# Optimization experiments

Measured on AMD Instinct MI355X. Metric: run time of the kernel, lower is better.

The kernel has to match this reference:

```python
import jax, jax.numpy as jnp
import numpy as np

N = 100000      # nodes
E = 50000       # hyperedges
NNZ = 1600000   # nonzeros in incidence matrix (avg 16 nodes/hyperedge)
C = 128         # in_channels
H = 256         # hidden_size


def setup_inputs() -> dict:
    key = jax.random.key(0)
    ks = jax.random.split(key, 8)
    x = jax.random.normal(ks[0], (N, C), dtype=jnp.float32)
    inc_rows = jax.random.randint(ks[1], (NNZ,), 0, E, dtype=jnp.int32)
    inc_cols = jax.random.randint(ks[2], (NNZ,), 0, N, dtype=jnp.int32)
    inc_vals = jax.random.uniform(ks[3], (NNZ,), dtype=jnp.float32)
    y = jax.random.randint(ks[4], (N,), 0, 10, dtype=jnp.int32)
    batch_0 = jnp.zeros((N,), dtype=jnp.int32)
    # Linear params (PyTorch Linear: y = x @ W.T + b; we store W pre-transposed as [C,H])
    s = 1.0 / np.sqrt(C)
    W0 = jax.random.uniform(ks[5], (C, H), dtype=jnp.float32, minval=-s, maxval=s)
    b0 = jnp.zeros((H,), dtype=jnp.float32)
    W1 = jax.random.uniform(ks[6], (C, H), dtype=jnp.float32, minval=-s, maxval=s)
    b1 = jnp.zeros((H,), dtype=jnp.float32)
    return {"x": x, "inc_rows": inc_rows, "inc_cols": inc_cols, "inc_vals": inc_vals,
            "y": y, "batch_0": batch_0, "W0": W0, "b0": b0, "W1": W1, "b1": b1}


def reference(x, inc_rows, inc_cols, inc_vals, y, batch_0, W0, b0, W1, b1):
    # sparse incidence @ x : gather node features per nnz, scale, scatter-add into hyperedges
    gathered = x[inc_cols] * inc_vals[:, None]                     # [NNZ, C]
    x1 = jax.ops.segment_sum(gathered, inc_rows, num_segments=E)   # [E, C]
    x0_out = jax.nn.relu(x @ W0 + b0)    # [N, H]
    x1_out = jax.nn.relu(x1 @ W1 + b1)   # [E, H]
    return (y, batch_0, x0_out, x1_out)
```

## Files before the change

kernel.cpp:

```cpp
#include <hip/hip_runtime.h>

#define N_NODES 100000
#define E_EDGES 50000
#define NNZ_CNT 1600000
#define C_IN 128
#define H_OUT 256
#define BKT 128
#define NB 391
#define RPB 4096

typedef __attribute__((ext_vector_type(8))) short short8;
typedef __attribute__((ext_vector_type(4))) float f32x4;

__device__ __forceinline__ ushort f2b(float f) {
  union { float f; uint u; } v; v.f = f;
  return (ushort)((v.u + 0x7FFFu + ((v.u >> 16) & 1u)) >> 16);
}
__device__ __forceinline__ float b2f(ushort u) {
  union { uint u; float f; } v; v.u = ((uint)u) << 16;
  return v.f;
}

__global__ __launch_bounds__(256) void init_kernel(
    const float* __restrict__ x, const int* __restrict__ y,
    const int* __restrict__ batch0, ushort* __restrict__ xb,
    float* __restrict__ out, int* __restrict__ chist, int nconv4) {
  int i = blockIdx.x * 256 + threadIdx.x;
  if (i < nconv4) {
    float4 v = ((const float4*)x)[i];
    ushort4 u;
    u.x = f2b(v.x); u.y = f2b(v.y); u.z = f2b(v.z); u.w = f2b(v.w);
    ((ushort4*)xb)[i] = u;
  }
  if (i < NB) chist[i] = 0;
  if (i < N_NODES) {
    out[i]           = (float)y[i];
    out[N_NODES + i] = (float)batch0[i];
  }
}

__global__ __launch_bounds__(256) void histc_kernel(
    const int* __restrict__ rows, int* __restrict__ chist) {
  __shared__ int h[NB];
  int t = threadIdx.x;
  for (int b = t; b < NB; b += 256) h[b] = 0;
  __syncthreads();
  int i0 = blockIdx.x * RPB;
  for (int k = 0; k < RPB / 256; ++k) {
    int i = i0 + k * 256 + t;
    if (i < NNZ_CNT) atomicAdd(&h[rows[i] >> 7], 1);
  }
  __syncthreads();
  for (int b = t; b < NB; b += 256)
    if (h[b]) atomicAdd(&chist[b], h[b]);
}

__global__ __launch_bounds__(512) void scanc_kernel(
    const int* __restrict__ chist, int* __restrict__ boff,
    int* __restrict__ gtail, int* __restrict__ eoff) {
  __shared__ int s[512];
  int t = threadIdx.x;
  int v = (t < NB) ? chist[t] : 0;
  s[t] = v;
  __syncthreads();
  for (int d = 1; d < 512; d <<= 1) {
    int u = (t >= d) ? s[t - d] : 0;
    __syncthreads();
    s[t] += u;
    __syncthreads();
  }
  if (t < NB) {
    int ex = s[t] - v;
    boff[t]  = ex;
    gtail[t] = ex;
  }
  if (t == 0) { boff[NB] = NNZ_CNT; eoff[NB * BKT] = NNZ_CNT; }
}

__global__ __launch_bounds__(256) void binpass_kernel(
    const int* __restrict__ rows, const int* __restrict__ cols,
    const float* __restrict__ vals, int* __restrict__ gtail,
    uint2* __restrict__ buf) {
  __shared__ int hist[NB], rnk[NB], base[NB];
  int t = threadIdx.x;
  for (int b = t; b < NB; b += 256) { hist[b] = 0; rnk[b] = 0; }
  __syncthreads();
  int i0 = blockIdx.x * RPB;
  for (int k = 0; k < RPB / 256; ++k) {
    int i = i0 + k * 256 + t;
    if (i < NNZ_CNT) atomicAdd(&hist[rows[i] >> 7], 1);
  }
  __syncthreads();
  for (int b = t; b < NB; b += 256) {
    int c = hist[b];
    base[b] = c ? atomicAdd(&gtail[b], c) : 0;
  }
  __syncthreads();
  for (int k = 0; k < RPB / 256; ++k) {
    int i = i0 + k * 256 + t;
    if (i < NNZ_CNT) {
      int r = rows[i];
      int b = r >> 7;
      int pos = base[b] + atomicAdd(&rnk[b], 1);
      buf[pos] = make_uint2(((uint)(r & (BKT - 1)) << 17) | (uint)cols[i],
                            __float_as_uint(vals[i]));
    }
  }
}

__global__ __launch_bounds__(256) void finepass_kernel(
    const uint2* __restrict__ buf, const int* __restrict__ boff,
    uint2* __restrict__ buf2, int* __restrict__ eoff) {
  __shared__ int lhist[BKT], lexc[BKT], lrnk[BKT];
  int t = threadIdx.x;
  int b = blockIdx.x;
  if (t < BKT) { lhist[t] = 0; lrnk[t] = 0; }
  __syncthreads();
  int start = boff[b], end = boff[b + 1];
  for (int i = start + t; i < end; i += 256)
    atomicAdd(&lhist[buf[i].x >> 17], 1);
  __syncthreads();
  if (t < BKT) lexc[t] = lhist[t];
  __syncthreads();
  for (int d = 1; d < BKT; d <<= 1) {
    int v = (t < BKT && t >= d) ? lexc[t - d] : 0;
    __syncthreads();
    if (t < BKT) lexc[t] += v;
    __syncthreads();
  }
  if (t < BKT) {
    int ex = lexc[t] - lhist[t];
    lexc[t] = ex;
    eoff[b * BKT + t] = start + ex;
  }
  __syncthreads();
  for (int i = start + t; i < end; i += 256) {
    uint2 rec = buf[i];
    int rl = rec.x >> 17;
    int r = atomicAdd(&lrnk[rl], 1);
    buf2[start + lexc[rl] + r] = rec;
  }
}

__global__ __launch_bounds__(128) void edge_reduce(
    const ushort* __restrict__ xb, const uint2* __restrict__ buf2,
    const int* __restrict__ eoff, ushort* __restrict__ x1b) {
  __shared__ uint2 meta[128];
  int e = blockIdx.x, t = threadIdx.x;
  int start = eoff[e], end = eoff[e + 1];
  float acc = 0.f;
  for (int base = start; base < end; base += 128) {
    int m = min(128, end - base);
    if (t < m) meta[t] = buf2[base + t];
    __syncthreads();
    for (int j = 0; j < m; ++j) {
      uint2 rec = meta[j];
      acc = fmaf(b2f(xb[(size_t)(rec.x & 0x1FFFFu) * C_IN + t]),
                 __uint_as_float(rec.y), acc);
    }
    __syncthreads();
  }
  x1b[(size_t)e * C_IN + t] = f2b(acc);
}

__global__ __launch_bounds__(256) void wprep_kernel(
    const float* __restrict__ W0, const float* __restrict__ W1,
    ushort* __restrict__ Wf) {
  int idx = blockIdx.x * 256 + threadIdx.x;
  if (idx >= 8192) return;
  const float* W = (idx & 4096) ? W1 : W0;
  int slot = idx & 4095;
  int nt = slot >> 8, ks = (slot >> 6) & 3, lane = slot & 63;
  int c  = nt * 16 + (lane & 15);
  int kb = ks * 32 + ((lane >> 4) << 3);
  short8 v;
#pragma unroll
  for (int j = 0; j < 8; ++j) v[j] = (short)f2b(W[(kb + j) * H_OUT + c]);
  ((short8*)Wf)[idx] = v;
}

__global__ __launch_bounds__(256) void gemm_mfma(
    const ushort* __restrict__ A, const ushort* __restrict__ Wf,
    const float* __restrict__ bias, float* __restrict__ out, int M) {
  int wave = threadIdx.x >> 6;
  int lane = threadIdx.x & 63;
  int wm = wave >> 1, wn = wave & 1;
  int r0 = blockIdx.x * 64 + wm * 32;

  int arow = lane & 15;
  int kgrp = lane >> 4;

  short8 a[2][4];
#pragma unroll
  for (int mt = 0; mt < 2; ++mt) {
    int row = min(r0 + mt * 16 + arow, M - 1);
    const ushort* ap = A + (size_t)row * C_IN + kgrp * 8;
#pragma unroll
    for (int ks = 0; ks < 4; ++ks)
      a[mt][ks] = *(const short8*)(ap + ks * 32);
  }

  f32x4 acc[2][8];
#pragma unroll
  for (int mt = 0; mt < 2; ++mt)
#pragma unroll
    for (int nt = 0; nt < 8; ++nt) acc[mt][nt] = (f32x4){0.f, 0.f, 0.f, 0.f};

#pragma unroll
  for (int nt = 0; nt < 8; ++nt) {
    int gnt = wn * 8 + nt;
    const short8* bp = (const short8*)Wf + (size_t)(gnt * 4) * 64 + lane;
#pragma unroll
    for (int ks = 0; ks < 4; ++ks) {
      short8 bfrag = bp[(size_t)ks * 64];
      acc[0][nt] = __builtin_amdgcn_mfma_f32_16x16x32_bf16(a[0][ks], bfrag, acc[0][nt], 0, 0, 0);
      acc[1][nt] = __builtin_amdgcn_mfma_f32_16x16x32_bf16(a[1][ks], bfrag, acc[1][nt], 0, 0, 0);
    }
  }

  int crow = kgrp * 4;
  int ccol = lane & 15;
#pragma unroll
  for (int mt = 0; mt < 2; ++mt) {
#pragma unroll
    for (int nt = 0; nt < 8; ++nt) {
      int col = wn * 128 + nt * 16 + ccol;
      float bb = bias[col];
#pragma unroll
      for (int reg = 0; reg < 4; ++reg) {
        int row = r0 + mt * 16 + crow + reg;
        if (row < M)
          out[(size_t)row * H_OUT + col] = fmaxf(acc[mt][nt][reg] + bb, 0.f);
      }
    }
  }
}

extern "C" void kernel_launch(void* const* d_in, const int* in_sizes, int n_in,
                              void* d_out, int out_size, void* d_ws, size_t ws_size,
                              hipStream_t stream) {
  const float* x        = (const float*)d_in[0];
  const int*   inc_rows = (const int*)d_in[1];
  const int*   inc_cols = (const int*)d_in[2];
  const float* inc_vals = (const float*)d_in[3];
  const int*   y        = (const int*)d_in[4];
  const int*   batch0   = (const int*)d_in[5];
  const float* W0       = (const float*)d_in[6];
  const float* b0       = (const float*)d_in[7];
  const float* W1       = (const float*)d_in[8];
  const float* b1       = (const float*)d_in[9];

  float* out = (float*)d_out;

  char* ws = (char*)d_ws;
  ushort* xb    = (ushort*)ws;  ws += (size_t)N_NODES * C_IN * 2;
  ushort* x1b   = (ushort*)ws;  ws += (size_t)E_EDGES * C_IN * 2;
  uint2*  buf   = (uint2*)ws;   ws += (size_t)NNZ_CNT * 8;
  uint2*  buf2  = (uint2*)ws;   ws += (size_t)NNZ_CNT * 8;
  ushort* Wf    = (ushort*)ws;  ws += (size_t)8192 * 8 * 2;
  int*    chist = (int*)ws;     ws += (size_t)NB * 4;
  int*    boff  = (int*)ws;     ws += (size_t)(NB + 1) * 4;
  int*    gtail = (int*)ws;     ws += (size_t)NB * 4;
  int*    eoff  = (int*)ws;

  const int nconv4 = N_NODES * C_IN / 4;
  const int nbin   = (NNZ_CNT + RPB - 1) / RPB;

  init_kernel<<<(nconv4 + 255) / 256, 256, 0, stream>>>(x, y, batch0, xb, out,
                                                        chist, nconv4);
  histc_kernel<<<nbin, 256, 0, stream>>>(inc_rows, chist);
  scanc_kernel<<<1, 512, 0, stream>>>(chist, boff, gtail, eoff);
  binpass_kernel<<<nbin, 256, 0, stream>>>(inc_rows, inc_cols, inc_vals,
                                           gtail, buf);
  finepass_kernel<<<NB, 256, 0, stream>>>(buf, boff, buf2, eoff);
  wprep_kernel<<<32, 256, 0, stream>>>(W0, W1, Wf);
  edge_reduce<<<E_EDGES, 128, 0, stream>>>(xb, buf2, eoff, x1b);

  float* x0_out = out + 2 * N_NODES;
  float* x1_out = out + 2 * N_NODES + (size_t)N_NODES * H_OUT;

  gemm_mfma<<<(N_NODES + 63) / 64, 256, 0, stream>>>(xb, Wf, b0, x0_out, N_NODES);
  gemm_mfma<<<(E_EDGES + 63) / 64, 256, 0, stream>>>(x1b, Wf + 8 * 4096, b1,
                                                     x1_out, E_EDGES);
}
```

Measured before the change: 216.3 us.

## Use wave-per-edge reduction, merge both GEMMs into one launch, cache rows in binpass

The edge reduction now assigns one 64-lane wave per hyperedge, each lane handling two channels via ushort2 loads. This drops the shared-memory staging and block-wide barriers of the old 128-thread-per-edge kernel. The two GEMM launches are merged into a single grid that dispatches by block index, which removes one launch and lets the tail of one GEMM overlap the other. Binpass keeps its row indices in registers instead of reloading them, and the histogram clear moves to a hipMemsetAsync. Each lane now reads metadata directly from global memory per nonzero, and register pressure in binpass goes up.

```diff
diff --git a/kernel.cpp b/kernel.cpp
--- a/kernel.cpp
+++ b/kernel.cpp
@@ -24,7 +24,7 @@
 __global__ __launch_bounds__(256) void init_kernel(
     const float* __restrict__ x, const int* __restrict__ y,
     const int* __restrict__ batch0, ushort* __restrict__ xb,
-    float* __restrict__ out, int* __restrict__ chist, int nconv4) {
+    float* __restrict__ out, int nconv4) {
   int i = blockIdx.x * 256 + threadIdx.x;
   if (i < nconv4) {
     float4 v = ((const float4*)x)[i];
@@ -32,7 +32,6 @@
     u.x = f2b(v.x); u.y = f2b(v.y); u.z = f2b(v.z); u.w = f2b(v.w);
     ((ushort4*)xb)[i] = u;
   }
-  if (i < NB) chist[i] = 0;
   if (i < N_NODES) {
     out[i]           = (float)y[i];
     out[N_NODES + i] = (float)batch0[i];
@@ -82,13 +81,17 @@
     const float* __restrict__ vals, int* __restrict__ gtail,
     uint2* __restrict__ buf) {
   __shared__ int hist[NB], rnk[NB], base[NB];
+  int rcache[RPB / 256];
   int t = threadIdx.x;
   for (int b = t; b < NB; b += 256) { hist[b] = 0; rnk[b] = 0; }
   __syncthreads();
   int i0 = blockIdx.x * RPB;
+#pragma unroll
   for (int k = 0; k < RPB / 256; ++k) {
     int i = i0 + k * 256 + t;
-    if (i < NNZ_CNT) atomicAdd(&hist[rows[i] >> 7], 1);
+    int r = (i < NNZ_CNT) ? rows[i] : -1;
+    rcache[k] = r;
+    if (r >= 0) atomicAdd(&hist[r >> 7], 1);
   }
   __syncthreads();
   for (int b = t; b < NB; b += 256) {
@@ -96,10 +99,11 @@
     base[b] = c ? atomicAdd(&gtail[b], c) : 0;
   }
   __syncthreads();
+#pragma unroll
   for (int k = 0; k < RPB / 256; ++k) {
-    int i = i0 + k * 256 + t;
-    if (i < NNZ_CNT) {
-      int r = rows[i];
+    int r = rcache[k];
+    if (r >= 0) {
+      int i = i0 + k * 256 + t;
       int b = r >> 7;
       int pos = base[b] + atomicAdd(&rnk[b], 1);
       buf[pos] = make_uint2(((uint)(r & (BKT - 1)) << 17) | (uint)cols[i],
@@ -142,25 +146,24 @@
   }
 }
 
-__global__ __launch_bounds__(128) void edge_reduce(
+__global__ __launch_bounds__(256) void edge_reduce(
     const ushort* __restrict__ xb, const uint2* __restrict__ buf2,
     const int* __restrict__ eoff, ushort* __restrict__ x1b) {
-  __shared__ uint2 meta[128];
-  int e = blockIdx.x, t = threadIdx.x;
+  int wave = threadIdx.x >> 6, lane = threadIdx.x & 63;
+  int e = blockIdx.x * 4 + wave;
+  if (e >= E_EDGES) return;
   int start = eoff[e], end = eoff[e + 1];
-  float acc = 0.f;
-  for (int base = start; base < end; base += 128) {
-    int m = min(128, end - base);
-    if (t < m) meta[t] = buf2[base + t];
-    __syncthreads();
-    for (int j = 0; j < m; ++j) {
-      uint2 rec = meta[j];
-      acc = fmaf(b2f(xb[(size_t)(rec.x & 0x1FFFFu) * C_IN + t]),
-                 __uint_as_float(rec.y), acc);
-    }
-    __syncthreads();
-  }
-  x1b[(size_t)e * C_IN + t] = f2b(acc);
+  float a0 = 0.f, a1 = 0.f;
+  for (int j = start; j < end; ++j) {
+    uint2 rec = buf2[j];
+    float v = __uint_as_float(rec.y);
+    ushort2 xv = *(const ushort2*)(xb + (size_t)(rec.x & 0x1FFFFu) * C_IN +
+                                   2 * lane);
+    a0 = fmaf(b2f(xv.x), v, a0);
+    a1 = fmaf(b2f(xv.y), v, a1);
+  }
+  uint lo = f2b(a0), hi = f2b(a1);
+  ((uint*)x1b)[(size_t)e * 64 + lane] = lo | (hi << 16);
 }
 
 __global__ __launch_bounds__(256) void wprep_kernel(
@@ -179,13 +182,13 @@
   ((short8*)Wf)[idx] = v;
 }
 
-__global__ __launch_bounds__(256) void gemm_mfma(
+__device__ __forceinline__ void gemm_body(
     const ushort* __restrict__ A, const ushort* __restrict__ Wf,
-    const float* __restrict__ bias, float* __restrict__ out, int M) {
+    const float* __restrict__ bias, float* __restrict__ out, int M, int bid) {
   int wave = threadIdx.x >> 6;
   int lane = threadIdx.x & 63;
   int wm = wave >> 1, wn = wave & 1;
-  int r0 = blockIdx.x * 64 + wm * 32;
+  int r0 = bid * 64 + wm * 32;
 
   int arow = lane & 15;
   int kgrp = lane >> 4;
@@ -234,6 +237,18 @@
       }
     }
   }
+}
+
+__global__ __launch_bounds__(256) void gemm_dual(
+    const ushort* __restrict__ A0, const ushort* __restrict__ A1,
+    const ushort* __restrict__ Wf, const float* __restrict__ bias0,
+    const float* __restrict__ bias1, float* __restrict__ out0,
+    float* __restrict__ out1, int nb0) {
+  int bid = blockIdx.x;
+  if (bid < nb0)
+    gemm_body(A0, Wf, bias0, out0, N_NODES, bid);
+  else
+    gemm_body(A1, Wf + 8 * 4096, bias1, out1, E_EDGES, bid - nb0);
 }
 
 extern "C" void kernel_launch(void* const* d_in, const int* in_sizes, int n_in,
@@ -265,21 +280,23 @@
 
   const int nconv4 = N_NODES * C_IN / 4;
   const int nbin   = (NNZ_CNT + RPB - 1) / RPB;
-
+  const int nb0    = (N_NODES + 63) / 64;
+  const int nb1    = (E_EDGES + 63) / 64;
+
+  wprep_kernel<<<32, 256, 0, stream>>>(W0, W1, Wf);
+  hipMemsetAsync(chist, 0, (size_t)NB * 4, stream);
   init_kernel<<<(nconv4 + 255) / 256, 256, 0, stream>>>(x, y, batch0, xb, out,
-                                                        chist, nconv4);
+                                                        nconv4);
   histc_kernel<<<nbin, 256, 0, stream>>>(inc_rows, chist);
   scanc_kernel<<<1, 512, 0, stream>>>(chist, boff, gtail, eoff);
   binpass_kernel<<<nbin, 256, 0, stream>>>(inc_rows, inc_cols, inc_vals,
                                            gtail, buf);
   finepass_kernel<<<NB, 256, 0, stream>>>(buf, boff, buf2, eoff);
-  wprep_kernel<<<32, 256, 0, stream>>>(W0, W1, Wf);
-  edge_reduce<<<E_EDGES, 128, 0, stream>>>(xb, buf2, eoff, x1b);
+  edge_reduce<<<(E_EDGES + 3) / 4, 256, 0, stream>>>(xb, buf2, eoff, x1b);
 
   float* x0_out = out + 2 * N_NODES;
   float* x1_out = out + 2 * N_NODES + (size_t)N_NODES * H_OUT;
 
-  gemm_mfma<<<(N_NODES + 63) / 64, 256, 0, stream>>>(xb, Wf, b0, x0_out, N_NODES);
-  gemm_mfma<<<(E_EDGES + 63) / 64, 256, 0, stream>>>(x1b, Wf + 8 * 4096, b1,
-                                                     x1_out, E_EDGES);
-}
+  gemm_dual<<<nb0 + nb1, 256, 0, stream>>>(xb, x1b, Wf, b0, b1,
+                                           x0_out, x1_out, nb0);
+}
```

After: 304.2 us. 40.7% more time.
